# Kernel optimization log

Measured on AMD Instinct MI355X. Metric: run time of the kernel, lower is better.

The kernel has to match this reference:

```python
import jax, jax.numpy as jnp
import numpy as np

GAMMA = 0.96875      # retention decay, 1 - 2**-5
GROUPS = 8           # config.group_norm_num
EPS = 1e-6           # config.retention_group_norm_eps


def _get_D(T, dtype):
    # D[n, m] = gamma**(n-m) for n >= m else 0 (causal exponential decay)
    n = jnp.arange(T)[:, None]
    m = jnp.arange(T)[None, :]
    log_g = jnp.log(jnp.asarray(GAMMA, dtype))
    # where-select avoids inf*0 NaNs for n < m (matches D[D != D] = 0)
    return jnp.where(n >= m, jnp.exp((n - m).astype(dtype) * log_g),
                     jnp.zeros((), dtype))


def _group_norm(x, w, b):
    # x: (N, C); torch.nn.GroupNorm semantics (biased variance, affine)
    N, C = x.shape
    xg = x.reshape(N, GROUPS, C // GROUPS)
    mu = xg.mean(-1, keepdims=True)
    var = xg.var(-1, keepdims=True)
    xn = ((xg - mu) * jax.lax.rsqrt(var + EPS)).reshape(N, C)
    return xn * w + b


def setup_inputs() -> dict:
    key = jax.random.key(0)
    k0, k1, k2, k3, k4 = jax.random.split(key, 5)
    B, T, C = 2, 8192, 64
    Q_in = jax.random.normal(k0, (B, T, C), jnp.float32)
    W_Q = jax.random.normal(k1, (C, C), jnp.float32) / C
    W_K = jax.random.normal(k2, (C, C), jnp.float32) / C
    W_V = jax.random.normal(k3, (C, C), jnp.float32) / C
    gn_weight = 1.0 + 0.02 * jax.random.normal(k4, (C,), jnp.float32)
    gn_bias = jnp.zeros((C,), jnp.float32)
    return {"Q_in": Q_in, "W_Q": W_Q, "W_K": W_K, "W_V": W_V,
            "gn_weight": gn_weight, "gn_bias": gn_bias}


def reference(Q_in, W_Q, W_K, W_V, gn_weight, gn_bias):
    B, T, C = Q_in.shape
    # _qkv with KV_in=None, act='none'
    Q = Q_in @ W_Q
    K = Q_in @ W_K
    V = Q_in @ W_V
    # retention scores with multiplicative causal decay mask
    QK = jnp.einsum("btc,bsc->bts", Q, K) * _get_D(T, Q.dtype)[None]
    out = jnp.einsum("bts,bsc->btc", QK, V)  # (B, T, C)
    # _out: dropout(p=0) -> GroupNorm over flattened (B*T, C) -> transpose+view
    out = _group_norm(out.reshape(-1, C), gn_weight, gn_bias).reshape(B, T, C)
    out = jnp.swapaxes(out, -2, -1).reshape(B, T, C)  # faithful to .transpose().view()
    return out
```

## Files before the change

### kernel.cpp

```cpp
#include <hip/hip_runtime.h>


constexpr int SEQ = 8192;
constexpr int CH  = 64;
constexpr float LOG2G = -0.045803690f;

typedef __attribute__((ext_vector_type(8))) _Float16 half8;
typedef __attribute__((ext_vector_type(4))) float    f32x4;

__device__ inline unsigned short f2h(float x) {
    _Float16 h = (_Float16)x;
    return __builtin_bit_cast(unsigned short, h);
}

__global__ __launch_bounds__(256) void qkv_kernel(
    const float* __restrict__ Xin, const float* __restrict__ Wq,
    const float* __restrict__ Wk, const float* __restrict__ Wv,
    unsigned short* __restrict__ Qh, unsigned short* __restrict__ Kh,
    unsigned short* __restrict__ Vt)
{
    __shared__ unsigned short sWt[3][64][72];
    const int tid = threadIdx.x;
    const size_t row0 = (size_t)blockIdx.x * 64;
    const int b  = (int)(row0 >> 13);
    const int t0 = (int)(row0 & (SEQ - 1));

    {
        const int c  = tid & 63;
        const int k0 = (tid >> 6) * 2;
        #pragma unroll
        for (int m = 0; m < 3; ++m) {
            const float* W = (m == 0) ? Wq : ((m == 1) ? Wk : Wv);
            #pragma unroll
            for (int it = 0; it < 8; ++it) {
                const int k = k0 + it * 8;
                const unsigned lo = f2h(W[k * 64 + c]);
                const unsigned hi = f2h(W[(k + 1) * 64 + c]);
                *(unsigned int*)&sWt[m][c][k] = lo | (hi << 16);
            }
        }
    }

    const int l15 = tid & 15, q4 = (tid >> 4) & 3, wvi = tid >> 6;

    half8 xf[2];
    {
        const float* Xp = Xin + (row0 + (size_t)(wvi * 16 + l15)) * 64;
        #pragma unroll
        for (int h = 0; h < 2; ++h) {
            const f32x4 a  = *(const f32x4*)(Xp + h * 32 + q4 * 8);
            const f32x4 bb = *(const f32x4*)(Xp + h * 32 + q4 * 8 + 4);
            half8 t;
            t[0] = (_Float16)a[0];  t[1] = (_Float16)a[1];
            t[2] = (_Float16)a[2];  t[3] = (_Float16)a[3];
            t[4] = (_Float16)bb[0]; t[5] = (_Float16)bb[1];
            t[6] = (_Float16)bb[2]; t[7] = (_Float16)bb[3];
            xf[h] = t;
        }
    }
    __syncthreads();

    const int trow = (int)row0 + wvi * 16;
    #pragma unroll
    for (int m = 0; m < 2; ++m) {
        unsigned short* O = (m == 0) ? Qh : Kh;
        #pragma unroll
        for (int ct = 0; ct < 4; ++ct) {
            const half8 wf0 = *(const half8*)&sWt[m][ct * 16 + l15][q4 * 8];
            const half8 wf1 = *(const half8*)&sWt[m][ct * 16 + l15][32 + q4 * 8];
            f32x4 d = {0.f, 0.f, 0.f, 0.f};
            d = __builtin_amdgcn_mfma_f32_16x16x32_f16(xf[0], wf0, d, 0, 0, 0);
            d = __builtin_amdgcn_mfma_f32_16x16x32_f16(xf[1], wf1, d, 0, 0, 0);
            #pragma unroll
            for (int i = 0; i < 4; ++i)
                O[(size_t)(trow + q4 * 4 + i) * 64 + ct * 16 + l15] = f2h(d[i]);
        }
    }
    #pragma unroll
    for (int mt = 0; mt < 4; ++mt) {
        const half8 wf0 = *(const half8*)&sWt[2][mt * 16 + l15][q4 * 8];
        const half8 wf1 = *(const half8*)&sWt[2][mt * 16 + l15][32 + q4 * 8];
        f32x4 d = {0.f, 0.f, 0.f, 0.f};
        d = __builtin_amdgcn_mfma_f32_16x16x32_f16(wf0, xf[0], d, 0, 0, 0);
        d = __builtin_amdgcn_mfma_f32_16x16x32_f16(wf1, xf[1], d, 0, 0, 0);
        #pragma unroll
        for (int i = 0; i < 4; ++i)
            Vt[(size_t)(b * 64 + mt * 16 + q4 * 4 + i) * SEQ + t0 + wvi * 16 + l15] = f2h(d[i]);
    }
}

__global__ __launch_bounds__(128, 1) void attn_kernel(
    const unsigned short* __restrict__ Qh, const unsigned short* __restrict__ Kh,
    const unsigned short* __restrict__ Vt,
    const float* __restrict__ gnw, const float* __restrict__ gnb,
    float* __restrict__ out)
{
    __shared__ unsigned short sS[2][16][88];
    __shared__ float sO[2][16][68];
    __shared__ float sGW[64], sGB[64];

    const int tid  = threadIdx.x;
    const int wvi  = tid >> 6;
    const int lane = tid & 63;
    const int l15  = lane & 15, q4 = lane >> 4;
    const int tile = blockIdx.x * 2 + wvi;
    const int b    = tile >> 9;
    const int t0   = (tile & 511) << 4;

    if (tid < 64) { sGW[tid] = gnw[tid]; sGB[tid] = gnb[tid]; }
    __syncthreads();

    const unsigned short* Qp = Qh + (size_t)(b * SEQ + t0 + l15) * 64 + q4 * 8;
    const half8 qf0 = *(const half8*)Qp;
    const half8 qf1 = *(const half8*)(Qp + 32);

    float grs[4][4];
    #pragma unroll
    for (int st = 0; st < 4; ++st) {
        #pragma unroll
        for (int i = 0; i < 4; ++i)
            grs[st][i] = exp2f((float)(l15 - (st * 16 + q4 * 4 + i)) * LOG2G);
    }

    f32x4 acc[4];
    #pragma unroll
    for (int ct = 0; ct < 4; ++ct) acc[ct] = (f32x4){0.f, 0.f, 0.f, 0.f};

    const int cs_hi = (t0 + 15) >> 6;
    const int cs_lo = (cs_hi >= 16) ? (cs_hi - 16) : 0;

    const unsigned short* Kbase = Kh + (size_t)b * SEQ * 64;
    const unsigned short* Vbase = Vt + (size_t)b * 64 * SEQ;

    half8 kA[4][2], vA[4][2], kB[4][2], vB[4][2];

    auto loadKV = [&](int cs, half8 (&kf)[4][2], half8 (&vf)[4][2]) {
        const int s0 = cs << 6;
        #pragma unroll
        for (int st = 0; st < 4; ++st) {
            const unsigned short* p = Kbase + (size_t)(s0 + st * 16 + l15) * 64 + q4 * 8;
            kf[st][0] = *(const half8*)p;
            kf[st][1] = *(const half8*)(p + 32);
        }
        #pragma unroll
        for (int ct = 0; ct < 4; ++ct) {
            const unsigned short* p = Vbase + (size_t)(ct * 16 + l15) * SEQ + s0 + q4 * 8;
            vf[ct][0] = *(const half8*)p;
            vf[ct][1] = *(const half8*)(p + 32);
        }
    };

    auto body = [&](half8 (&kc)[4][2], half8 (&vc)[4][2],
                    half8 (&kn)[4][2], half8 (&vn)[4][2], int cs) {
        const int s0 = cs << 6;
        f32x4 sv[4];
        #pragma unroll
        for (int st = 0; st < 4; ++st) {
            f32x4 s = {0.f, 0.f, 0.f, 0.f};
            s = __builtin_amdgcn_mfma_f32_16x16x32_f16(kc[st][0], qf0, s, 0, 0, 0);
            s = __builtin_amdgcn_mfma_f32_16x16x32_f16(kc[st][1], qf1, s, 0, 0, 0);
            sv[st] = s;
        }
        if (cs < cs_hi) loadKV(cs + 1, kn, vn);
        const float gbase = exp2f((float)(t0 - s0) * LOG2G);
        if (s0 + 63 <= t0) {
            #pragma unroll
            for (int st = 0; st < 4; ++st) {
                const unsigned u0 = (unsigned)f2h(sv[st][0] * (gbase * grs[st][0]))
                                  | ((unsigned)f2h(sv[st][1] * (gbase * grs[st][1])) << 16);
                const unsigned u1 = (unsigned)f2h(sv[st][2] * (gbase * grs[st][2]))
                                  | ((unsigned)f2h(sv[st][3] * (gbase * grs[st][3])) << 16);
                unsigned int* p = (unsigned int*)&sS[wvi][l15][st * 16 + q4 * 4];
                p[0] = u0; p[1] = u1;
            }
        } else {
            const int dbase = t0 + l15 - s0;
            #pragma unroll
            for (int st = 0; st < 4; ++st) {
                float w[4];
                #pragma unroll
                for (int i = 0; i < 4; ++i) {
                    const int srel = st * 16 + q4 * 4 + i;
                    w[i] = (dbase - srel >= 0) ? gbase * grs[st][i] : 0.f;
                }
                const unsigned u0 = (unsigned)f2h(sv[st][0] * w[0])
                                  | ((unsigned)f2h(sv[st][1] * w[1]) << 16);
                const unsigned u1 = (unsigned)f2h(sv[st][2] * w[2])
                                  | ((unsigned)f2h(sv[st][3] * w[3]) << 16);
                unsigned int* p = (unsigned int*)&sS[wvi][l15][st * 16 + q4 * 4];
                p[0] = u0; p[1] = u1;
            }
        }
        const half8 af0 = *(const half8*)&sS[wvi][l15][q4 * 8];
        const half8 af1 = *(const half8*)&sS[wvi][l15][32 + q4 * 8];
        #pragma unroll
        for (int ct = 0; ct < 4; ++ct) {
            acc[ct] = __builtin_amdgcn_mfma_f32_16x16x32_f16(af0, vc[ct][0], acc[ct], 0, 0, 0);
            acc[ct] = __builtin_amdgcn_mfma_f32_16x16x32_f16(af1, vc[ct][1], acc[ct], 0, 0, 0);
        }
    };

    loadKV(cs_lo, kA, vA);
    int cs = cs_lo;
    while (true) {
        body(kA, vA, kB, vB, cs);
        if (++cs > cs_hi) break;
        body(kB, vB, kA, vA, cs);
        if (++cs > cs_hi) break;
    }

    #pragma unroll
    for (int ct = 0; ct < 4; ++ct) {
        #pragma unroll
        for (int i = 0; i < 4; ++i)
            sO[wvi][q4 * 4 + i][ct * 16 + l15] = acc[ct][i];
    }
    const int tt = lane >> 2, g2 = lane & 3;
    float x[16];
    #pragma unroll
    for (int j = 0; j < 4; ++j)
        *(f32x4*)&x[j * 4] = *(const f32x4*)&sO[wvi][tt][g2 * 16 + j * 4];
    #pragma unroll
    for (int gg = 0; gg < 2; ++gg) {
        float s = 0.f, ss = 0.f;
        #pragma unroll
        for (int j = 0; j < 8; ++j) { const float v = x[gg * 8 + j]; s += v; ss += v * v; }
        const float mu  = s * 0.125f;
        const float var = ss * 0.125f - mu * mu;
        const float rs  = rsqrtf(var + 1e-6f);
        #pragma unroll
        for (int j = 0; j < 8; ++j) {
            const int c = g2 * 16 + gg * 8 + j;
            x[gg * 8 + j] = (x[gg * 8 + j] - mu) * rs * sGW[c] + sGB[c];
        }
    }
    #pragma unroll
    for (int j = 0; j < 4; ++j)
        *(f32x4*)&sO[wvi][tt][g2 * 16 + j * 4] = *(f32x4*)&x[j * 4];
    #pragma unroll
    for (int k = 0; k < 16; ++k) {
        const int c = k * 4 + q4;
        out[(size_t)(b * 64 + c) * SEQ + t0 + l15] = sO[wvi][l15][c];
    }
}

extern "C" void kernel_launch(void* const* d_in, const int* in_sizes, int n_in,
                              void* d_out, int out_size, void* d_ws, size_t ws_size,
                              hipStream_t stream)
{
    const float* Xin = (const float*)d_in[0];
    const float* Wq  = (const float*)d_in[1];
    const float* Wk  = (const float*)d_in[2];
    const float* Wv  = (const float*)d_in[3];
    const float* gnw = (const float*)d_in[4];
    const float* gnb = (const float*)d_in[5];

    const size_t NROW = (size_t)2 * SEQ;
    unsigned short* Qh = (unsigned short*)d_ws;
    unsigned short* Kh = Qh + NROW * CH;
    unsigned short* Vt = Kh + NROW * CH;

    qkv_kernel<<<dim3(256), dim3(256), 0, stream>>>(Xin, Wq, Wk, Wv, Qh, Kh, Vt);
    attn_kernel<<<dim3(512), dim3(128), 0, stream>>>(Qh, Kh, Vt, gnw, gnb, (float*)d_out);
}
```

Baseline: 102.7 us.

## Split each query tile's decay window across two waves and shrink the window

Each block now handles a single 16-row query tile. Its two waves split the KV chunk range in half, and their partial accumulators are summed through LDS before the group norm and the transposed store. The grid doubles and launch bounds now allow two blocks per CU, which should improve occupancy and shorten each wave's serial loop. The retained decay window also shrinks from 16 to 10 chunks of 64 keys, which skips work whose weights fall below about 1e-9. That trades a little accuracy for fewer MFMA and load iterations, and adds two block barriers.

Result: faster. 93.14 us (-9.3%).

```diff
diff --git a/kernel.cpp b/kernel.cpp
--- a/kernel.cpp
+++ b/kernel.cpp
@@ -89,21 +89,21 @@
     }
 }
 
-__global__ __launch_bounds__(128, 1) void attn_kernel(
+__global__ __launch_bounds__(128, 2) void attn_kernel(
     const unsigned short* __restrict__ Qh, const unsigned short* __restrict__ Kh,
     const unsigned short* __restrict__ Vt,
     const float* __restrict__ gnw, const float* __restrict__ gnb,
     float* __restrict__ out)
 {
     __shared__ unsigned short sS[2][16][88];
-    __shared__ float sO[2][16][68];
+    __shared__ __align__(16) float sP[2][16][68];
     __shared__ float sGW[64], sGB[64];
 
     const int tid  = threadIdx.x;
     const int wvi  = tid >> 6;
     const int lane = tid & 63;
     const int l15  = lane & 15, q4 = lane >> 4;
-    const int tile = blockIdx.x * 2 + wvi;
+    const int tile = blockIdx.x;
     const int b    = tile >> 9;
     const int t0   = (tile & 511) << 4;
 
@@ -127,7 +127,11 @@
     for (int ct = 0; ct < 4; ++ct) acc[ct] = (f32x4){0.f, 0.f, 0.f, 0.f};
 
     const int cs_hi = (t0 + 15) >> 6;
-    const int cs_lo = (cs_hi >= 16) ? (cs_hi - 16) : 0;
+    const int cs_lo = (cs_hi >= 10) ? (cs_hi - 9) : 0;
+    const int n     = cs_hi - cs_lo + 1;
+    const int n0    = n >> 1;
+    const int myLo  = cs_lo + (wvi ? n0 : 0);
+    const int myHi  = wvi ? cs_hi : (cs_lo + n0 - 1);
 
     const unsigned short* Kbase = Kh + (size_t)b * SEQ * 64;
     const unsigned short* Vbase = Vt + (size_t)b * 64 * SEQ;
@@ -161,7 +165,7 @@
             s = __builtin_amdgcn_mfma_f32_16x16x32_f16(kc[st][1], qf1, s, 0, 0, 0);
             sv[st] = s;
         }
-        if (cs < cs_hi) loadKV(cs + 1, kn, vn);
+        if (cs < myHi) loadKV(cs + 1, kn, vn);
         const float gbase = exp2f((float)(t0 - s0) * LOG2G);
         if (s0 + 63 <= t0) {
             #pragma unroll
@@ -200,47 +204,55 @@
         }
     };
 
-    loadKV(cs_lo, kA, vA);
-    int cs = cs_lo;
-    while (true) {
-        body(kA, vA, kB, vB, cs);
-        if (++cs > cs_hi) break;
-        body(kB, vB, kA, vA, cs);
-        if (++cs > cs_hi) break;
+    if (myLo <= myHi) {
+        loadKV(myLo, kA, vA);
+        int cs = myLo;
+        while (true) {
+            body(kA, vA, kB, vB, cs);
+            if (++cs > myHi) break;
+            body(kB, vB, kA, vA, cs);
+            if (++cs > myHi) break;
+        }
     }
 
     #pragma unroll
     for (int ct = 0; ct < 4; ++ct) {
         #pragma unroll
         for (int i = 0; i < 4; ++i)
-            sO[wvi][q4 * 4 + i][ct * 16 + l15] = acc[ct][i];
-    }
-    const int tt = lane >> 2, g2 = lane & 3;
-    float x[16];
-    #pragma unroll
-    for (int j = 0; j < 4; ++j)
-        *(f32x4*)&x[j * 4] = *(const f32x4*)&sO[wvi][tt][g2 * 16 + j * 4];
-    #pragma unroll
-    for (int gg = 0; gg < 2; ++gg) {
-        float s = 0.f, ss = 0.f;
-        #pragma unroll
-        for (int j = 0; j < 8; ++j) { const float v = x[gg * 8 + j]; s += v; ss += v * v; }
-        const float mu  = s * 0.125f;
-        const float var = ss * 0.125f - mu * mu;
-        const float rs  = rsqrtf(var + 1e-6f);
-        #pragma unroll
-        for (int j = 0; j < 8; ++j) {
-            const int c = g2 * 16 + gg * 8 + j;
-            x[gg * 8 + j] = (x[gg * 8 + j] - mu) * rs * sGW[c] + sGB[c];
-        }
-    }
-    #pragma unroll
-    for (int j = 0; j < 4; ++j)
-        *(f32x4*)&sO[wvi][tt][g2 * 16 + j * 4] = *(f32x4*)&x[j * 4];
-    #pragma unroll
-    for (int k = 0; k < 16; ++k) {
-        const int c = k * 4 + q4;
-        out[(size_t)(b * 64 + c) * SEQ + t0 + l15] = sO[wvi][l15][c];
+            sP[wvi][q4 * 4 + i][ct * 16 + l15] = acc[ct][i];
+    }
+    __syncthreads();
+
+    const int tt = (wvi << 3) | (lane >> 3);
+    const int g  = lane & 7;
+    float x[8];
+    {
+        const f32x4 a0 = *(const f32x4*)&sP[0][tt][g * 8];
+        const f32x4 a1 = *(const f32x4*)&sP[0][tt][g * 8 + 4];
+        const f32x4 b0 = *(const f32x4*)&sP[1][tt][g * 8];
+        const f32x4 b1 = *(const f32x4*)&sP[1][tt][g * 8 + 4];
+        #pragma unroll
+        for (int j = 0; j < 4; ++j) { x[j] = a0[j] + b0[j]; x[4 + j] = a1[j] + b1[j]; }
+    }
+    float s = 0.f, ss = 0.f;
+    #pragma unroll
+    for (int j = 0; j < 8; ++j) { s += x[j]; ss += x[j] * x[j]; }
+    const float mu  = s * 0.125f;
+    const float var = ss * 0.125f - mu * mu;
+    const float rs  = rsqrtf(var + 1e-6f);
+    #pragma unroll
+    for (int j = 0; j < 8; ++j) {
+        const int c = g * 8 + j;
+        x[j] = (x[j] - mu) * rs * sGW[c] + sGB[c];
+    }
+    *(f32x4*)&sP[0][tt][g * 8]     = (f32x4){x[0], x[1], x[2], x[3]};
+    *(f32x4*)&sP[0][tt][g * 8 + 4] = (f32x4){x[4], x[5], x[6], x[7]};
+    __syncthreads();
+
+    #pragma unroll
+    for (int k2 = 0; k2 < 8; ++k2) {
+        const int c = ((wvi << 3) | k2) * 4 + q4;
+        out[(size_t)(b * 64 + c) * SEQ + t0 + l15] = sP[0][l15][c];
     }
 }
 
@@ -261,5 +273,5 @@
     unsigned short* Vt = Kh + NROW * CH;
 
     qkv_kernel<<<dim3(256), dim3(256), 0, stream>>>(Xin, Wq, Wk, Wv, Qh, Kh, Vt);
-    attn_kernel<<<dim3(512), dim3(128), 0, stream>>>(Qh, Kh, Vt, gnw, gnb, (float*)d_out);
-}
+    attn_kernel<<<dim3(1024), dim3(128), 0, stream>>>(Qh, Kh, Vt, gnw, gnb, (float*)d_out);
+}
```
